# Kernel optimization log

Hardware: AMD Instinct MI355X
Metric: run time of the kernel (lower is better)

Reference implementation:

```python
import jax, jax.numpy as jnp
import numpy as np

G, P, D, K = 64, 1024, 64, 6  # graphs, nodes/graph, features, knn k
N = G * P


def _lin_init(k, shape):
    s = 1.0 / np.sqrt(shape[0])
    return jax.random.uniform(k, shape, minval=-s, maxval=s, dtype=jnp.float32)


def setup_inputs() -> dict:
    key = jax.random.key(0)
    ks = jax.random.split(key, 16)
    return {
        "x": jax.random.normal(ks[0], (N, D), jnp.float32),
        "batchidxs": jnp.repeat(jnp.arange(G, dtype=jnp.int32), P),
        "pre_W1": _lin_init(ks[1], (D, D)),
        "pre_b1": _lin_init(ks[2], (D,)),
        "pre_a1": jnp.full((D,), 0.25, jnp.float32),
        "pre_W2": _lin_init(ks[3], (D, D)),
        "pre_b2": _lin_init(ks[4], (D,)),
        "pre_a2": jnp.full((D,), 0.25, jnp.float32),
        "bn_gamma": jnp.ones((D,), jnp.float32),
        "bn_beta": jnp.zeros((D,), jnp.float32),
        "act_a": jnp.full((D,), 0.25, jnp.float32),
        "conv_W": jax.random.normal(ks[5], (4, D, D), jnp.float32) / np.sqrt(D),
        "conv_b": jnp.zeros((4, D), jnp.float32),
        "ffn_W1": _lin_init(ks[6], (5 * D, 5 * D)),
        "ffn_b1": _lin_init(ks[7], (5 * D,)),
        "ffn_W2": _lin_init(ks[8], (5 * D, 1)),
        "ffn_b2": _lin_init(ks[9], (1,)),
    }


def _prelu(x, a):
    return jnp.where(x >= 0, x, a * x)


def _knn_edges(x):
    """knn_graph with k=K per graph (equal-sized graphs). Returns (src, dst) global idx."""
    xg = x.reshape(G, P, D)

    def knn_one(pts):  # [P, D] -> [P, K] local neighbor idx
        sq = jnp.sum(pts * pts, axis=-1)
        d2 = sq[:, None] + sq[None, :] - 2.0 * (pts @ pts.T)
        d2 = d2 + jnp.eye(P, dtype=d2.dtype) * 1e10  # exclude self-loop
        _, idx = jax.lax.top_k(-d2, K)
        return idx

    nbr = jax.vmap(knn_one)(xg)  # [G, P, K]
    offs = (jnp.arange(G, dtype=nbr.dtype) * P)[:, None, None]
    src = (nbr + offs).reshape(-1)  # source (neighbor) nodes x_j
    dst = jnp.broadcast_to(jnp.arange(P, dtype=nbr.dtype)[None, :, None] + offs,
                           (G, P, K)).reshape(-1)  # target (query) nodes
    return src, dst


def reference(x, batchidxs, pre_W1, pre_b1, pre_a1, pre_W2, pre_b2, pre_a2,
              bn_gamma, bn_beta, act_a, conv_W, conv_b,
              ffn_W1, ffn_b1, ffn_W2, ffn_b2):
    src, dst = _knn_edges(x)

    # pre_nn: Linear -> PReLU -> Linear -> PReLU -> BatchNorm (training stats)
    h = _prelu(x @ pre_W1 + pre_b1, pre_a1)
    h = _prelu(h @ pre_W2 + pre_b2, pre_a2)
    mu = jnp.mean(h, axis=0)
    var = jnp.var(h, axis=0)
    h = (h - mu) * jax.lax.rsqrt(var + 1e-5) * bn_gamma + bn_beta

    xs = [h]
    for i in range(4):
        msg = h[src] @ conv_W[i] + conv_b[i]            # gather + transform [E, D]
        aggr = jax.ops.segment_sum(msg, dst, num_segments=N)  # scatter-add
        h = _prelu(aggr + h, act_a)                     # shared PReLU act
        xs.append(h)

    hc = jnp.concatenate(xs, axis=-1)                   # JumpingKnowledge 'cat' [N, 5D]
    pooled = jax.ops.segment_sum(hc, batchidxs, num_segments=G)  # global_add_pool [G, 5D]

    # hlv_dnn FFN(5D -> 1): Linear -> LeakyReLU -> Linear
    z = pooled @ ffn_W1 + ffn_b1
    z = jnp.where(z >= 0, z, 0.01 * z)
    return z @ ffn_W2 + ffn_b2
```

## Files before the change

### kernel.cpp

```cpp
#include <hip/hip_runtime.h>


typedef float4 f4;
typedef unsigned short ushort;
typedef unsigned int uint;
typedef _Float16 f16;
typedef _Float16 f16x8 __attribute__((ext_vector_type(8)));
typedef float f32x16 __attribute__((ext_vector_type(16)));

#define Z16 {0.f,0.f,0.f,0.f,0.f,0.f,0.f,0.f,0.f,0.f,0.f,0.f,0.f,0.f,0.f,0.f}

union HU { f16 h; ushort u; };
__device__ __forceinline__ ushort f2h_u(float f) { HU x; x.h = (f16)f; return x.u; }
__device__ __forceinline__ f16 u2h(ushort u) { HU x; x.u = u; return x.h; }

__device__ __forceinline__ uint med3u(uint a, uint b, uint c) {
  uint d;
  asm("v_med3_u32 %0, %1, %2, %3" : "=v"(d) : "v"(a), "v"(b), "v"(c));
  return d;
}

#define INSM(x) do { \
  m5 = med3u((x), m4, m5); \
  m4 = med3u((x), m3, m4); \
  m3 = med3u((x), m2, m3); \
  m2 = med3u((x), m1, m2); \
  m1 = med3u((x), m0, m1); \
  m0 = max(m0, (x)); \
} while (0)

__global__ void kwprep(const float* __restrict__ W1, const float* __restrict__ W2,
                       const float* __restrict__ convW, ushort* __restrict__ wt) {
  const int m = blockIdx.x;
  const float* src = (m == 0) ? W1 : (m == 1) ? W2 : convW + (m - 2) * 4096;
  ushort* dst = wt + m * 4096;
  for (int i = threadIdx.x; i < 4096; i += 256) {
    int k = i >> 6, n = i & 63;
    dst[n * 64 + k] = f2h_u(src[i]);
  }
}

__global__ __launch_bounds__(256, 4) void kknn(const ushort* __restrict__ xf16,
                                               const uint* __restrict__ sq2,
                                               int* __restrict__ nbr) {
  __shared__ uint skey[4][32][6];
  const int tid = threadIdx.x;
  const int lane = tid & 63;
  const int w = tid >> 6;
  const int q = lane & 31;
  const int h = lane >> 5;
  const int g = blockIdx.x >> 5;
  const int qtile = blockIdx.x & 31;
  const int gbase = g << 10;
  const int qloc = qtile * 32 + q;
  const int qglob = gbase + qloc;

  f16x8 Q0, Q1, Q2, Q3;
  {
    const ushort* qp = xf16 + (size_t)qglob * 64 + 8 * h;
    Q0 = *(const f16x8*)(qp);       Q1 = *(const f16x8*)(qp + 16);
    Q2 = *(const f16x8*)(qp + 32);  Q3 = *(const f16x8*)(qp + 48);
  }
  f16x8 Bsq = {(f16)0, (f16)0, (f16)0, (f16)0, (f16)0, (f16)0, (f16)0, (f16)0};
  if (h == 0) { Bsq[0] = (f16)1.0f; Bsq[1] = (f16)1.0f; }

  uint m0 = 0, m1 = 0, m2 = 0, m3 = 0, m4 = 0, m5 = 0;

  for (int cc = 0; cc < 8; ++cc) {
    const int cg = w * 8 + cc;
    const int cb = gbase + cg * 32;
    const ushort* cp = xf16 + (size_t)(cb + q) * 64 + 8 * h;
    f16x8 A0 = *(const f16x8*)(cp);       f16x8 A1 = *(const f16x8*)(cp + 16);
    f16x8 A2 = *(const f16x8*)(cp + 32);  f16x8 A3 = *(const f16x8*)(cp + 48);
    uint sv = sq2[cb + q];
    f16x8 Asq = {(f16)0, (f16)0, (f16)0, (f16)0, (f16)0, (f16)0, (f16)0, (f16)0};
    if (h == 0) { Asq[0] = u2h((ushort)(sv & 0xffffu)); Asq[1] = u2h((ushort)(sv >> 16)); }

    f32x16 acc = {1536.f,1536.f,1536.f,1536.f,1536.f,1536.f,1536.f,1536.f,
                  1536.f,1536.f,1536.f,1536.f,1536.f,1536.f,1536.f,1536.f};
    acc = __builtin_amdgcn_mfma_f32_32x32x16_f16(A0, Q0, acc, 0, 0, 0);
    acc = __builtin_amdgcn_mfma_f32_32x32x16_f16(A1, Q1, acc, 0, 0, 0);
    acc = __builtin_amdgcn_mfma_f32_32x32x16_f16(A2, Q2, acc, 0, 0, 0);
    acc = __builtin_amdgcn_mfma_f32_32x32x16_f16(A3, Q3, acc, 0, 0, 0);
    acc = __builtin_amdgcn_mfma_f32_32x32x16_f16(Asq, Bsq, acc, 0, 0, 0);

    const int cl0 = cg * 32 + 4 * h;
    const uint kb = (uint)(1023 - cl0);
    if (cg == qtile) {
#pragma unroll
      for (int r = 0; r < 16; ++r) {
        const int pat = (r & 3) + 8 * (r >> 2);
        uint u = __float_as_uint(acc[r]);
        uint key = (((u << 9) & 0xFFFFFC00u) | kb) - (uint)pat;
        if (cl0 + pat == qloc) key = 0u;
        INSM(key);
      }
    } else {
#pragma unroll
      for (int r = 0; r < 16; ++r) {
        const int pat = (r & 3) + 8 * (r >> 2);
        uint u = __float_as_uint(acc[r]);
        uint key = (((u << 9) & 0xFFFFFC00u) | kb) - (uint)pat;
        INSM(key);
      }
    }
  }

  {
    uint p0 = (uint)__shfl_xor((int)m0, 32, 64);
    uint p1 = (uint)__shfl_xor((int)m1, 32, 64);
    uint p2 = (uint)__shfl_xor((int)m2, 32, 64);
    uint p3 = (uint)__shfl_xor((int)m3, 32, 64);
    uint p4 = (uint)__shfl_xor((int)m4, 32, 64);
    uint p5 = (uint)__shfl_xor((int)m5, 32, 64);
    INSM(p0); INSM(p1); INSM(p2); INSM(p3); INSM(p4); INSM(p5);
  }
  if (h == 0) {
    skey[w][q][0] = m0; skey[w][q][1] = m1; skey[w][q][2] = m2;
    skey[w][q][3] = m3; skey[w][q][4] = m4; skey[w][q][5] = m5;
  }
  __syncthreads();

  if (tid < 32) {
    uint m0 = skey[0][tid][0], m1 = skey[0][tid][1], m2 = skey[0][tid][2];
    uint m3 = skey[0][tid][3], m4 = skey[0][tid][4], m5 = skey[0][tid][5];
#pragma unroll
    for (int ww = 1; ww < 4; ++ww)
#pragma unroll
      for (int k = 0; k < 6; ++k)
        INSM(skey[ww][tid][k]);
    const int ob = (gbase + qtile * 32 + tid) * 6;
    nbr[ob + 0] = gbase + 1023 - (int)(m0 & 1023u);
    nbr[ob + 1] = gbase + 1023 - (int)(m1 & 1023u);
    nbr[ob + 2] = gbase + 1023 - (int)(m2 & 1023u);
    nbr[ob + 3] = gbase + 1023 - (int)(m3 & 1023u);
    nbr[ob + 4] = gbase + 1023 - (int)(m4 & 1023u);
    nbr[ob + 5] = gbase + 1023 - (int)(m5 & 1023u);
  }
}

__global__ __launch_bounds__(256) void kpre(
    const float* __restrict__ x, const ushort* __restrict__ w1t,
    const float* __restrict__ b1, const float* __restrict__ p1,
    const ushort* __restrict__ w2t, const float* __restrict__ b2,
    const float* __restrict__ p2, ushort* __restrict__ hout,
    float* __restrict__ gsumg, float* __restrict__ gsq,
    ushort* __restrict__ xf16, uint* __restrict__ sq2) {
  __shared__ ushort tile[4][32][72];
  __shared__ float ls[64], lq[64];
  const int tid = threadIdx.x, lane = tid & 63, w = tid >> 6;
  const int q = lane & 31, h = lane >> 5;
  const int rbase = blockIdx.x * 128 + w * 32;
  const int row = rbase + q;
  const int g = blockIdx.x >> 3;
  if (tid < 64) { ls[tid] = 0.f; lq[tid] = 0.f; }
  __syncthreads();

  f16x8 Ax[4]; float ssq = 0.f;
  const float* xp = x + (size_t)row * 64 + 8 * h;
  ushort* xo = xf16 + (size_t)row * 64 + 8 * h;
#pragma unroll
  for (int ks = 0; ks < 4; ++ks) {
    f4 a = *(const f4*)(xp + 16 * ks);
    f4 b = *(const f4*)(xp + 16 * ks + 4);
    f16x8 f;
    f[0] = (f16)a.x; f[1] = (f16)a.y; f[2] = (f16)a.z; f[3] = (f16)a.w;
    f[4] = (f16)b.x; f[5] = (f16)b.y; f[6] = (f16)b.z; f[7] = (f16)b.w;
    Ax[ks] = f;
    *(f16x8*)(xo + 16 * ks) = f;
    ssq += a.x*a.x + a.y*a.y + a.z*a.z + a.w*a.w + b.x*b.x + b.y*b.y + b.z*b.z + b.w*b.w;
  }
  ssq += __shfl_xor(ssq, 32, 64);
  if (h == 0) {
    float mm = -0.5f * ssq;
    ushort u1 = f2h_u(mm); HU t1; t1.u = u1;
    ushort u2 = f2h_u(mm - (float)t1.h);
    sq2[row] = (uint)u1 | ((uint)u2 << 16);
  }

  f32x16 c0 = Z16, c1 = Z16;
#pragma unroll
  for (int ks = 0; ks < 4; ++ks) {
    f16x8 B0 = *(const f16x8*)(w1t + q * 64 + 16 * ks + 8 * h);
    f16x8 B1 = *(const f16x8*)(w1t + (q + 32) * 64 + 16 * ks + 8 * h);
    c0 = __builtin_amdgcn_mfma_f32_32x32x16_f16(Ax[ks], B0, c0, 0, 0, 0);
    c1 = __builtin_amdgcn_mfma_f32_32x32x16_f16(Ax[ks], B1, c1, 0, 0, 0);
  }
  {
    const float bb0 = b1[q], aa0 = p1[q], bb1 = b1[q + 32], aa1 = p1[q + 32];
#pragma unroll
    for (int r = 0; r < 16; ++r) {
      const int nd = (r & 3) + 8 * (r >> 2) + 4 * h;
      float v0 = c0[r] + bb0; v0 = v0 >= 0.f ? v0 : aa0 * v0;
      float v1 = c1[r] + bb1; v1 = v1 >= 0.f ? v1 : aa1 * v1;
      tile[w][nd][q] = f2h_u(v0);
      tile[w][nd][q + 32] = f2h_u(v1);
    }
  }
  f16x8 Ah[4];
#pragma unroll
  for (int ks = 0; ks < 4; ++ks)
    Ah[ks] = *(const f16x8*)&tile[w][q][16 * ks + 8 * h];

  f32x16 d0 = Z16, d1 = Z16;
#pragma unroll
  for (int ks = 0; ks < 4; ++ks) {
    f16x8 B0 = *(const f16x8*)(w2t + q * 64 + 16 * ks + 8 * h);
    f16x8 B1 = *(const f16x8*)(w2t + (q + 32) * 64 + 16 * ks + 8 * h);
    d0 = __builtin_amdgcn_mfma_f32_32x32x16_f16(Ah[ks], B0, d0, 0, 0, 0);
    d1 = __builtin_amdgcn_mfma_f32_32x32x16_f16(Ah[ks], B1, d1, 0, 0, 0);
  }
  {
    const float bb0 = b2[q], aa0 = p2[q], bb1 = b2[q + 32], aa1 = p2[q + 32];
    float s0 = 0.f, q0 = 0.f, s1 = 0.f, q1 = 0.f;
#pragma unroll
    for (int r = 0; r < 16; ++r) {
      const int nd = (r & 3) + 8 * (r >> 2) + 4 * h;
      float v0 = d0[r] + bb0; v0 = v0 >= 0.f ? v0 : aa0 * v0;
      float v1 = d1[r] + bb1; v1 = v1 >= 0.f ? v1 : aa1 * v1;
      ushort u0 = f2h_u(v0), u1 = f2h_u(v1);
      HU t0, t1; t0.u = u0; t1.u = u1;
      float r0 = (float)t0.h, r1 = (float)t1.h;
      s0 += r0; q0 += r0 * r0; s1 += r1; q1 += r1 * r1;
      tile[w][nd][q] = u0;
      tile[w][nd][q + 32] = u1;
    }
    s0 += __shfl_xor(s0, 32, 64); q0 += __shfl_xor(q0, 32, 64);
    s1 += __shfl_xor(s1, 32, 64); q1 += __shfl_xor(q1, 32, 64);
    if (h == 0) {
      atomicAdd(&ls[q], s0); atomicAdd(&lq[q], q0);
      atomicAdd(&ls[q + 32], s1); atomicAdd(&lq[q + 32], q1);
    }
  }
  ushort* ho = hout + (size_t)row * 64 + 8 * h;
#pragma unroll
  for (int ks = 0; ks < 4; ++ks) {
    f16x8 v = *(const f16x8*)&tile[w][q][16 * ks + 8 * h];
    *(f16x8*)(ho + 16 * ks) = v;
  }
  __syncthreads();
  if (tid < 64) {
    atomicAdd(&gsumg[g * 64 + tid], ls[tid]);
    atomicAdd(&gsq[tid], lq[tid]);
  }
}

__global__ void kfin(const float* __restrict__ gsumg, const float* __restrict__ gsq,
                     const float* __restrict__ gamma, const float* __restrict__ beta,
                     float* __restrict__ scale, float* __restrict__ shift,
                     float* __restrict__ pooled) {
  const int g = blockIdx.x, f = threadIdx.x;
  float s = 0.f;
  for (int g2 = 0; g2 < 64; ++g2) s += gsumg[g2 * 64 + f];
  float mu = s * (1.f / 65536.f);
  float var = gsq[f] * (1.f / 65536.f) - mu * mu;
  float sc = gamma[f] * rsqrtf(var + 1e-5f);
  float sh = beta[f] - mu * sc;
  pooled[g * 320 + f] = sc * gsumg[g * 64 + f] + 1024.f * sh;
  if (g == 0) { scale[f] = sc; shift[f] = sh; }
}

template <int BN>
__global__ __launch_bounds__(256) void kconv(
    const ushort* __restrict__ hIn, ushort* __restrict__ hOut,
    const int* __restrict__ nbr, const ushort* __restrict__ wt,
    const float* __restrict__ bias, const float* __restrict__ act,
    const float* __restrict__ scale, const float* __restrict__ shift,
    float* __restrict__ pooled, int stageoff) {
  __shared__ ushort tile[4][32][72];
  __shared__ float pool[64];
  const int tid = threadIdx.x, lane = tid & 63, w = tid >> 6;
  const int q = lane & 31, h = lane >> 5;
  const int nbase = blockIdx.x * 128 + w * 32;
  const int node = nbase + q;
  const int g = blockIdx.x >> 3;
  if (tid < 64) pool[tid] = 0.f;
  __syncthreads();

  const int* np = nbr + (size_t)node * 6;
  const int j0 = np[0], j1 = np[1], j2 = np[2], j3 = np[3], j4 = np[4], j5 = np[5];

  f16x8 Af[4];
#pragma unroll
  for (int ks = 0; ks < 4; ++ks) {
    const int off = 16 * ks + 8 * h;
    float s0=0.f,s1=0.f,s2=0.f,s3=0.f,s4=0.f,s5=0.f,s6=0.f,s7=0.f;
#define ACC6(J) { f16x8 v = *(const f16x8*)(hIn + (size_t)(J) * 64 + off); \
    s0 += (float)v[0]; s1 += (float)v[1]; s2 += (float)v[2]; s3 += (float)v[3]; \
    s4 += (float)v[4]; s5 += (float)v[5]; s6 += (float)v[6]; s7 += (float)v[7]; }
    ACC6(j0) ACC6(j1) ACC6(j2) ACC6(j3) ACC6(j4) ACC6(j5)
#undef ACC6
    if (BN) {
      f4 sa = *(const f4*)(scale + off), sb = *(const f4*)(scale + off + 4);
      f4 ha = *(const f4*)(shift + off), hb = *(const f4*)(shift + off + 4);
      s0 = s0*sa.x + 6.f*ha.x; s1 = s1*sa.y + 6.f*ha.y;
      s2 = s2*sa.z + 6.f*ha.z; s3 = s3*sa.w + 6.f*ha.w;
      s4 = s4*sb.x + 6.f*hb.x; s5 = s5*sb.y + 6.f*hb.y;
      s6 = s6*sb.z + 6.f*hb.z; s7 = s7*sb.w + 6.f*hb.w;
    }
    f16x8 f;
    f[0]=(f16)s0; f[1]=(f16)s1; f[2]=(f16)s2; f[3]=(f16)s3;
    f[4]=(f16)s4; f[5]=(f16)s5; f[6]=(f16)s6; f[7]=(f16)s7;
    Af[ks] = f;
  }

  f32x16 c0 = Z16, c1 = Z16;
#pragma unroll
  for (int ks = 0; ks < 4; ++ks) {
    f16x8 B0 = *(const f16x8*)(wt + q * 64 + 16 * ks + 8 * h);
    f16x8 B1 = *(const f16x8*)(wt + (q + 32) * 64 + 16 * ks + 8 * h);
    c0 = __builtin_amdgcn_mfma_f32_32x32x16_f16(Af[ks], B0, c0, 0, 0, 0);
    c1 = __builtin_amdgcn_mfma_f32_32x32x16_f16(Af[ks], B1, c1, 0, 0, 0);
  }
  {
    const float bb0 = 6.f * bias[q], bb1 = 6.f * bias[q + 32];
#pragma unroll
    for (int r = 0; r < 16; ++r) {
      const int nd = (r & 3) + 8 * (r >> 2) + 4 * h;
      tile[w][nd][q] = f2h_u(c0[r] + bb0);
      tile[w][nd][q + 32] = f2h_u(c1[r] + bb1);
    }
  }

  const int a = lane >> 3, b = lane & 7;
  f4 aa0 = *(const f4*)(act + 8 * b), aa1 = *(const f4*)(act + 8 * b + 4);
  f4 rs0, rs1, rh0, rh1;
  if (BN) {
    rs0 = *(const f4*)(scale + 8 * b); rs1 = *(const f4*)(scale + 8 * b + 4);
    rh0 = *(const f4*)(shift + 8 * b); rh1 = *(const f4*)(shift + 8 * b + 4);
  }
  f4 ps0 = {0.f,0.f,0.f,0.f}, ps1 = ps0;
#pragma unroll
  for (int r = 0; r < 4; ++r) {
    const int nd = 4 * a + r;
    const size_t gn = (size_t)(nbase + nd) * 64 + 8 * b;
    f16x8 z = *(const f16x8*)&tile[w][nd][8 * b];
    f16x8 ro = *(const f16x8*)(hIn + gn);
    float v0 = (float)z[0] + (BN ? rs0.x * (float)ro[0] + rh0.x : (float)ro[0]);
    float v1 = (float)z[1] + (BN ? rs0.y * (float)ro[1] + rh0.y : (float)ro[1]);
    float v2 = (float)z[2] + (BN ? rs0.z * (float)ro[2] + rh0.z : (float)ro[2]);
    float v3 = (float)z[3] + (BN ? rs0.w * (float)ro[3] + rh0.w : (float)ro[3]);
    float v4 = (float)z[4] + (BN ? rs1.x * (float)ro[4] + rh1.x : (float)ro[4]);
    float v5 = (float)z[5] + (BN ? rs1.y * (float)ro[5] + rh1.y : (float)ro[5]);
    float v6 = (float)z[6] + (BN ? rs1.z * (float)ro[6] + rh1.z : (float)ro[6]);
    float v7 = (float)z[7] + (BN ? rs1.w * (float)ro[7] + rh1.w : (float)ro[7]);
    v0 = v0 >= 0.f ? v0 : aa0.x * v0;  v1 = v1 >= 0.f ? v1 : aa0.y * v1;
    v2 = v2 >= 0.f ? v2 : aa0.z * v2;  v3 = v3 >= 0.f ? v3 : aa0.w * v3;
    v4 = v4 >= 0.f ? v4 : aa1.x * v4;  v5 = v5 >= 0.f ? v5 : aa1.y * v5;
    v6 = v6 >= 0.f ? v6 : aa1.z * v6;  v7 = v7 >= 0.f ? v7 : aa1.w * v7;
    ps0.x += v0; ps0.y += v1; ps0.z += v2; ps0.w += v3;
    ps1.x += v4; ps1.y += v5; ps1.z += v6; ps1.w += v7;
    f16x8 o;
    o[0]=(f16)v0; o[1]=(f16)v1; o[2]=(f16)v2; o[3]=(f16)v3;
    o[4]=(f16)v4; o[5]=(f16)v5; o[6]=(f16)v6; o[7]=(f16)v7;
    *(f16x8*)(hOut + gn) = o;
  }
#pragma unroll
  for (int m = 8; m <= 32; m <<= 1) {
    ps0.x += __shfl_xor(ps0.x, m, 64); ps0.y += __shfl_xor(ps0.y, m, 64);
    ps0.z += __shfl_xor(ps0.z, m, 64); ps0.w += __shfl_xor(ps0.w, m, 64);
    ps1.x += __shfl_xor(ps1.x, m, 64); ps1.y += __shfl_xor(ps1.y, m, 64);
    ps1.z += __shfl_xor(ps1.z, m, 64); ps1.w += __shfl_xor(ps1.w, m, 64);
  }
  if (a == 0) {
    atomicAdd(&pool[8 * b + 0], ps0.x); atomicAdd(&pool[8 * b + 1], ps0.y);
    atomicAdd(&pool[8 * b + 2], ps0.z); atomicAdd(&pool[8 * b + 3], ps0.w);
    atomicAdd(&pool[8 * b + 4], ps1.x); atomicAdd(&pool[8 * b + 5], ps1.y);
    atomicAdd(&pool[8 * b + 6], ps1.z); atomicAdd(&pool[8 * b + 7], ps1.w);
  }
  __syncthreads();
  if (tid < 64) atomicAdd(&pooled[g * 320 + stageoff + tid], pool[tid]);
}

__global__ __launch_bounds__(256) void kffn(const float* __restrict__ pooled,
    const float* __restrict__ W1, const float* __restrict__ b1,
    const float* __restrict__ W2, const float* __restrict__ b2,
    float* __restrict__ out) {
  __shared__ float pg[320];
  __shared__ float z1[320];
  __shared__ float red[4];
  const int g = blockIdx.x, tid = threadIdx.x;
  for (int i = tid; i < 320; i += 256) pg[i] = pooled[g * 320 + i];
  __syncthreads();
  for (int o = tid; o < 320; o += 256) {
    float acc = b1[o];
    for (int d = 0; d < 320; ++d) acc += pg[d] * W1[d * 320 + o];
    z1[o] = acc >= 0.f ? acc : 0.01f * acc;
  }
  __syncthreads();
  float p = 0.f;
  for (int o = tid; o < 320; o += 256) p += z1[o] * W2[o];
#pragma unroll
  for (int m = 32; m; m >>= 1) p += __shfl_xor(p, m, 64);
  if ((tid & 63) == 0) red[tid >> 6] = p;
  __syncthreads();
  if (tid == 0) out[g] = red[0] + red[1] + red[2] + red[3] + b2[0];
}

extern "C" void kernel_launch(void* const* d_in, const int* in_sizes, int n_in,
                              void* d_out, int out_size, void* d_ws, size_t ws_size,
                              hipStream_t stream) {
  const float* x        = (const float*)d_in[0];
  const float* pre_W1   = (const float*)d_in[2];
  const float* pre_b1   = (const float*)d_in[3];
  const float* pre_a1   = (const float*)d_in[4];
  const float* pre_W2   = (const float*)d_in[5];
  const float* pre_b2   = (const float*)d_in[6];
  const float* pre_a2   = (const float*)d_in[7];
  const float* bn_gamma = (const float*)d_in[8];
  const float* bn_beta  = (const float*)d_in[9];
  const float* act_a    = (const float*)d_in[10];
  const float* conv_W   = (const float*)d_in[11];
  const float* conv_b   = (const float*)d_in[12];
  const float* ffn_W1   = (const float*)d_in[13];
  const float* ffn_b1   = (const float*)d_in[14];
  const float* ffn_W2   = (const float*)d_in[15];
  const float* ffn_b2   = (const float*)d_in[16];
  float* out = (float*)d_out;

  ushort* hA16 = (ushort*)d_ws;
  ushort* hB16 = hA16 + 4194304;
  ushort* xf16 = hB16 + 4194304;
  uint*   sq2  = (uint*)(xf16 + 4194304);
  int*    nbr  = (int*)(sq2 + 65536);
  ushort* wt   = (ushort*)(nbr + 393216);
  float* stats = (float*)(wt + 24576);
  float* gsq    = stats;
  float* gsumg  = stats + 64;
  float* scale  = stats + 64 + 4096;
  float* shift  = stats + 64 + 4096 + 64;
  float* pooled = stats + 64 + 4096 + 128;

  hipMemsetAsync(stats, 0, (64 + 4096 + 128 + 64 * 320) * sizeof(float), stream);

  kwprep<<<6, 256, 0, stream>>>(pre_W1, pre_W2, conv_W, wt);
  kpre  <<<512, 256, 0, stream>>>(x, wt, pre_b1, pre_a1, wt + 4096, pre_b2, pre_a2,
                                  hA16, gsumg, gsq, xf16, sq2);
  kknn  <<<2048, 256, 0, stream>>>(xf16, sq2, nbr);
  kfin  <<<64, 64, 0, stream>>>(gsumg, gsq, bn_gamma, bn_beta, scale, shift, pooled);
  kconv<1><<<512, 256, 0, stream>>>(hA16, hB16, nbr, wt + 2*4096, conv_b,       act_a, scale, shift, pooled, 64);
  kconv<0><<<512, 256, 0, stream>>>(hB16, hA16, nbr, wt + 3*4096, conv_b + 64,  act_a, scale, shift, pooled, 128);
  kconv<0><<<512, 256, 0, stream>>>(hA16, hB16, nbr, wt + 4*4096, conv_b + 128, act_a, scale, shift, pooled, 192);
  kconv<0><<<512, 256, 0, stream>>>(hB16, hA16, nbr, wt + 5*4096, conv_b + 192, act_a, scale, shift, pooled, 256);
  kffn  <<<64, 256, 0, stream>>>(pooled, ffn_W1, ffn_b1, ffn_W2, ffn_b2, out);
}
```

Measured before the change: 244.7 us.

## Fuse four graph-conv layers into one per-graph kernel with LDS-resident features

Replaces four separate conv launches with one kernel that runs one 1024-thread block per graph. The block loads the graph's BN-normalized features into shared memory once, then runs all four layers with neighbor gathers and residual reads served from LDS. This removes the global round trips of intermediate features and three launches. In exchange only 64 blocks run, which leaves most CUs idle, and each block uses about 147KB of LDS.

After: 251.9 us. 1.03x slower.

```diff
diff --git a/kernel.cpp b/kernel.cpp
--- a/kernel.cpp
+++ b/kernel.cpp
@@ -260,116 +260,113 @@
   if (g == 0) { scale[f] = sc; shift[f] = sh; }
 }
 
-template <int BN>
-__global__ __launch_bounds__(256) void kconv(
-    const ushort* __restrict__ hIn, ushort* __restrict__ hOut,
-    const int* __restrict__ nbr, const ushort* __restrict__ wt,
-    const float* __restrict__ bias, const float* __restrict__ act,
-    const float* __restrict__ scale, const float* __restrict__ shift,
-    float* __restrict__ pooled, int stageoff) {
-  __shared__ ushort tile[4][32][72];
+__global__ __launch_bounds__(1024, 4) void kconv4(
+    const ushort* __restrict__ hIn, const int* __restrict__ nbr,
+    const ushort* __restrict__ wt, const float* __restrict__ cb,
+    const float* __restrict__ act, const float* __restrict__ scale,
+    const float* __restrict__ shift, float* __restrict__ pooled) {
+  __shared__ ushort hl[1024][72];
   __shared__ float pool[64];
   const int tid = threadIdx.x, lane = tid & 63, w = tid >> 6;
   const int q = lane & 31, h = lane >> 5;
-  const int nbase = blockIdx.x * 128 + w * 32;
-  const int node = nbase + q;
-  const int g = blockIdx.x >> 3;
+  const int g = blockIdx.x;
+  const size_t gb = (size_t)g * 65536;
+
+  {
+    const int seg = tid & 7, r0 = tid >> 3;
+    const f4 sa = *(const f4*)(scale + seg * 8);
+    const f4 sb = *(const f4*)(scale + seg * 8 + 4);
+    const f4 ha = *(const f4*)(shift + seg * 8);
+    const f4 hb = *(const f4*)(shift + seg * 8 + 4);
+#pragma unroll
+    for (int p = 0; p < 8; ++p) {
+      const int row = r0 + p * 128;
+      f16x8 v = *(const f16x8*)(hIn + gb + (size_t)row * 64 + seg * 8);
+      f16x8 o;
+      o[0] = (f16)((float)v[0] * sa.x + ha.x);
+      o[1] = (f16)((float)v[1] * sa.y + ha.y);
+      o[2] = (f16)((float)v[2] * sa.z + ha.z);
+      o[3] = (f16)((float)v[3] * sa.w + ha.w);
+      o[4] = (f16)((float)v[4] * sb.x + hb.x);
+      o[5] = (f16)((float)v[5] * sb.y + hb.y);
+      o[6] = (f16)((float)v[6] * sb.z + hb.z);
+      o[7] = (f16)((float)v[7] * sb.w + hb.w);
+      *(f16x8*)&hl[row][seg * 8] = o;
+    }
+  }
   if (tid < 64) pool[tid] = 0.f;
-  __syncthreads();
-
-  const int* np = nbr + (size_t)node * 6;
-  const int j0 = np[0], j1 = np[1], j2 = np[2], j3 = np[3], j4 = np[4], j5 = np[5];
-
-  f16x8 Af[4];
-#pragma unroll
-  for (int ks = 0; ks < 4; ++ks) {
-    const int off = 16 * ks + 8 * h;
-    float s0=0.f,s1=0.f,s2=0.f,s3=0.f,s4=0.f,s5=0.f,s6=0.f,s7=0.f;
-#define ACC6(J) { f16x8 v = *(const f16x8*)(hIn + (size_t)(J) * 64 + off); \
-    s0 += (float)v[0]; s1 += (float)v[1]; s2 += (float)v[2]; s3 += (float)v[3]; \
-    s4 += (float)v[4]; s5 += (float)v[5]; s6 += (float)v[6]; s7 += (float)v[7]; }
-    ACC6(j0) ACC6(j1) ACC6(j2) ACC6(j3) ACC6(j4) ACC6(j5)
-#undef ACC6
-    if (BN) {
-      f4 sa = *(const f4*)(scale + off), sb = *(const f4*)(scale + off + 4);
-      f4 ha = *(const f4*)(shift + off), hb = *(const f4*)(shift + off + 4);
-      s0 = s0*sa.x + 6.f*ha.x; s1 = s1*sa.y + 6.f*ha.y;
-      s2 = s2*sa.z + 6.f*ha.z; s3 = s3*sa.w + 6.f*ha.w;
-      s4 = s4*sb.x + 6.f*hb.x; s5 = s5*sb.y + 6.f*hb.y;
-      s6 = s6*sb.z + 6.f*hb.z; s7 = s7*sb.w + 6.f*hb.w;
-    }
-    f16x8 f;
-    f[0]=(f16)s0; f[1]=(f16)s1; f[2]=(f16)s2; f[3]=(f16)s3;
-    f[4]=(f16)s4; f[5]=(f16)s5; f[6]=(f16)s6; f[7]=(f16)s7;
-    Af[ks] = f;
-  }
-
-  f32x16 c0 = Z16, c1 = Z16;
-#pragma unroll
-  for (int ks = 0; ks < 4; ++ks) {
-    f16x8 B0 = *(const f16x8*)(wt + q * 64 + 16 * ks + 8 * h);
-    f16x8 B1 = *(const f16x8*)(wt + (q + 32) * 64 + 16 * ks + 8 * h);
-    c0 = __builtin_amdgcn_mfma_f32_32x32x16_f16(Af[ks], B0, c0, 0, 0, 0);
-    c1 = __builtin_amdgcn_mfma_f32_32x32x16_f16(Af[ks], B1, c1, 0, 0, 0);
-  }
-  {
-    const float bb0 = 6.f * bias[q], bb1 = 6.f * bias[q + 32];
-#pragma unroll
-    for (int r = 0; r < 16; ++r) {
-      const int nd = (r & 3) + 8 * (r >> 2) + 4 * h;
-      tile[w][nd][q] = f2h_u(c0[r] + bb0);
-      tile[w][nd][q + 32] = f2h_u(c1[r] + bb1);
-    }
-  }
-
-  const int a = lane >> 3, b = lane & 7;
-  f4 aa0 = *(const f4*)(act + 8 * b), aa1 = *(const f4*)(act + 8 * b + 4);
-  f4 rs0, rs1, rh0, rh1;
-  if (BN) {
-    rs0 = *(const f4*)(scale + 8 * b); rs1 = *(const f4*)(scale + 8 * b + 4);
-    rh0 = *(const f4*)(shift + 8 * b); rh1 = *(const f4*)(shift + 8 * b + 4);
-  }
-  f4 ps0 = {0.f,0.f,0.f,0.f}, ps1 = ps0;
-#pragma unroll
-  for (int r = 0; r < 4; ++r) {
-    const int nd = 4 * a + r;
-    const size_t gn = (size_t)(nbase + nd) * 64 + 8 * b;
-    f16x8 z = *(const f16x8*)&tile[w][nd][8 * b];
-    f16x8 ro = *(const f16x8*)(hIn + gn);
-    float v0 = (float)z[0] + (BN ? rs0.x * (float)ro[0] + rh0.x : (float)ro[0]);
-    float v1 = (float)z[1] + (BN ? rs0.y * (float)ro[1] + rh0.y : (float)ro[1]);
-    float v2 = (float)z[2] + (BN ? rs0.z * (float)ro[2] + rh0.z : (float)ro[2]);
-    float v3 = (float)z[3] + (BN ? rs0.w * (float)ro[3] + rh0.w : (float)ro[3]);
-    float v4 = (float)z[4] + (BN ? rs1.x * (float)ro[4] + rh1.x : (float)ro[4]);
-    float v5 = (float)z[5] + (BN ? rs1.y * (float)ro[5] + rh1.y : (float)ro[5]);
-    float v6 = (float)z[6] + (BN ? rs1.z * (float)ro[6] + rh1.z : (float)ro[6]);
-    float v7 = (float)z[7] + (BN ? rs1.w * (float)ro[7] + rh1.w : (float)ro[7]);
-    v0 = v0 >= 0.f ? v0 : aa0.x * v0;  v1 = v1 >= 0.f ? v1 : aa0.y * v1;
-    v2 = v2 >= 0.f ? v2 : aa0.z * v2;  v3 = v3 >= 0.f ? v3 : aa0.w * v3;
-    v4 = v4 >= 0.f ? v4 : aa1.x * v4;  v5 = v5 >= 0.f ? v5 : aa1.y * v5;
-    v6 = v6 >= 0.f ? v6 : aa1.z * v6;  v7 = v7 >= 0.f ? v7 : aa1.w * v7;
-    ps0.x += v0; ps0.y += v1; ps0.z += v2; ps0.w += v3;
-    ps1.x += v4; ps1.y += v5; ps1.z += v6; ps1.w += v7;
-    f16x8 o;
-    o[0]=(f16)v0; o[1]=(f16)v1; o[2]=(f16)v2; o[3]=(f16)v3;
-    o[4]=(f16)v4; o[5]=(f16)v5; o[6]=(f16)v6; o[7]=(f16)v7;
-    *(f16x8*)(hOut + gn) = o;
-  }
-#pragma unroll
-  for (int m = 8; m <= 32; m <<= 1) {
-    ps0.x += __shfl_xor(ps0.x, m, 64); ps0.y += __shfl_xor(ps0.y, m, 64);
-    ps0.z += __shfl_xor(ps0.z, m, 64); ps0.w += __shfl_xor(ps0.w, m, 64);
-    ps1.x += __shfl_xor(ps1.x, m, 64); ps1.y += __shfl_xor(ps1.y, m, 64);
-    ps1.z += __shfl_xor(ps1.z, m, 64); ps1.w += __shfl_xor(ps1.w, m, 64);
-  }
-  if (a == 0) {
-    atomicAdd(&pool[8 * b + 0], ps0.x); atomicAdd(&pool[8 * b + 1], ps0.y);
-    atomicAdd(&pool[8 * b + 2], ps0.z); atomicAdd(&pool[8 * b + 3], ps0.w);
-    atomicAdd(&pool[8 * b + 4], ps1.x); atomicAdd(&pool[8 * b + 5], ps1.y);
-    atomicAdd(&pool[8 * b + 6], ps1.z); atomicAdd(&pool[8 * b + 7], ps1.w);
-  }
-  __syncthreads();
-  if (tid < 64) atomicAdd(&pooled[g * 320 + stageoff + tid], pool[tid]);
+
+  const int nb0 = w * 64, nb1 = nb0 + 32;
+  int n0[6], n1[6];
+  {
+    const int* p0 = nbr + (size_t)(g * 1024 + nb0 + q) * 6;
+    const int* p1 = p0 + 32 * 6;
+#pragma unroll
+    for (int k = 0; k < 6; ++k) { n0[k] = p0[k] & 1023; n1[k] = p1[k] & 1023; }
+  }
+  __syncthreads();
+
+  for (int l = 0; l < 4; ++l) {
+    const ushort* wl = wt + (2 + l) * 4096;
+    const float bb0 = 6.f * cb[l * 64 + q], bb1 = 6.f * cb[l * 64 + q + 32];
+    const float av0 = act[q], av1 = act[q + 32];
+    uint o0[2][8], o1[2][8];
+#pragma unroll
+    for (int t = 0; t < 2; ++t) {
+      const int nb = t ? nb1 : nb0;
+      const int* nn = t ? n1 : n0;
+      f32x16 c0 = Z16, c1 = Z16;
+#pragma unroll
+      for (int ks = 0; ks < 4; ++ks) {
+        const int off = 16 * ks + 8 * h;
+        float s0=0.f,s1=0.f,s2=0.f,s3=0.f,s4=0.f,s5=0.f,s6=0.f,s7=0.f;
+#pragma unroll
+        for (int k = 0; k < 6; ++k) {
+          f16x8 v = *(const f16x8*)&hl[nn[k]][off];
+          s0 += (float)v[0]; s1 += (float)v[1]; s2 += (float)v[2]; s3 += (float)v[3];
+          s4 += (float)v[4]; s5 += (float)v[5]; s6 += (float)v[6]; s7 += (float)v[7];
+        }
+        f16x8 Af;
+        Af[0]=(f16)s0; Af[1]=(f16)s1; Af[2]=(f16)s2; Af[3]=(f16)s3;
+        Af[4]=(f16)s4; Af[5]=(f16)s5; Af[6]=(f16)s6; Af[7]=(f16)s7;
+        f16x8 B0 = *(const f16x8*)(wl + q * 64 + off);
+        f16x8 B1 = *(const f16x8*)(wl + (q + 32) * 64 + off);
+        c0 = __builtin_amdgcn_mfma_f32_32x32x16_f16(Af, B0, c0, 0, 0, 0);
+        c1 = __builtin_amdgcn_mfma_f32_32x32x16_f16(Af, B1, c1, 0, 0, 0);
+      }
+      float p0s = 0.f, p1s = 0.f;
+#pragma unroll
+      for (int r = 0; r < 16; ++r) {
+        const int nd = nb + (r & 3) + 8 * (r >> 2) + 4 * h;
+        float r0 = (float)u2h(hl[nd][q]);
+        float r1 = (float)u2h(hl[nd][q + 32]);
+        float v0 = c0[r] + bb0 + r0; v0 = v0 >= 0.f ? v0 : av0 * v0;
+        float v1 = c1[r] + bb1 + r1; v1 = v1 >= 0.f ? v1 : av1 * v1;
+        p0s += v0; p1s += v1;
+        uint u0 = (uint)f2h_u(v0), u1 = (uint)f2h_u(v1);
+        if (r & 1) { o0[t][r >> 1] |= u0 << 16; o1[t][r >> 1] |= u1 << 16; }
+        else       { o0[t][r >> 1] = u0;        o1[t][r >> 1] = u1; }
+      }
+      atomicAdd(&pool[q], p0s);
+      atomicAdd(&pool[q + 32], p1s);
+    }
+    __syncthreads();
+#pragma unroll
+    for (int t = 0; t < 2; ++t) {
+      const int nb = t ? nb1 : nb0;
+#pragma unroll
+      for (int r = 0; r < 16; ++r) {
+        const int nd = nb + (r & 3) + 8 * (r >> 2) + 4 * h;
+        hl[nd][q]      = (ushort)(o0[t][r >> 1] >> (16 * (r & 1)));
+        hl[nd][q + 32] = (ushort)(o1[t][r >> 1] >> (16 * (r & 1)));
+      }
+    }
+    if (tid < 64) {
+      atomicAdd(&pooled[g * 320 + 64 * (l + 1) + tid], pool[tid]);
+      pool[tid] = 0.f;
+    }
+    __syncthreads();
+  }
 }
 
 __global__ __launch_bounds__(256) void kffn(const float* __restrict__ pooled,
@@ -419,8 +416,7 @@
   float* out = (float*)d_out;
 
   ushort* hA16 = (ushort*)d_ws;
-  ushort* hB16 = hA16 + 4194304;
-  ushort* xf16 = hB16 + 4194304;
+  ushort* xf16 = hA16 + 4194304;
   uint*   sq2  = (uint*)(xf16 + 4194304);
   int*    nbr  = (int*)(sq2 + 65536);
   ushort* wt   = (ushort*)(nbr + 393216);
@@ -438,9 +434,6 @@
                                   hA16, gsumg, gsq, xf16, sq2);
   kknn  <<<2048, 256, 0, stream>>>(xf16, sq2, nbr);
   kfin  <<<64, 64, 0, stream>>>(gsumg, gsq, bn_gamma, bn_beta, scale, shift, pooled);
-  kconv<1><<<512, 256, 0, stream>>>(hA16, hB16, nbr, wt + 2*4096, conv_b,       act_a, scale, shift, pooled, 64);
-  kconv<0><<<512, 256, 0, stream>>>(hB16, hA16, nbr, wt + 3*4096, conv_b + 64,  act_a, scale, shift, pooled, 128);
-  kconv<0><<<512, 256, 0, stream>>>(hA16, hB16, nbr, wt + 4*4096, conv_b + 128, act_a, scale, shift, pooled, 192);
-  kconv<0><<<512, 256, 0, stream>>>(hB16, hA16, nbr, wt + 5*4096, conv_b + 192, act_a, scale, shift, pooled, 256);
+  kconv4<<<64, 1024, 0, stream>>>(hA16, nbr, wt, conv_b, act_a, scale, shift, pooled);
   kffn  <<<64, 256, 0, stream>>>(pooled, ffn_W1, ffn_b1, ffn_W2, ffn_b2, out);
 }
```
